# Performance work log

Hardware: AMD Instinct MI355X
Metric: run time of the kernel (lower is better)

The kernel has to match this reference:

```python
import jax, jax.numpy as jnp
import numpy as np
from jax import lax

B = 512
MBD_B, MBD_C = 64, 16
FEAT = 40 * 4 * 4  # 640


def _conv(x, w, b):
    y = lax.conv_general_dilated(x, w, (1, 1), 'VALID',
                                 dimension_numbers=('NCHW', 'OIHW', 'NCHW'))
    return y + b[None, :, None, None]


def _maxpool2(x):
    return lax.reduce_window(x, -jnp.inf, lax.max,
                             (1, 1, 2, 2), (1, 1, 2, 2), 'VALID')


def setup_inputs() -> dict:
    key = jax.random.key(0)
    ks = jax.random.split(key, 10)
    def he(k, shape, fan_in):
        return jax.random.normal(k, shape, dtype=jnp.float32) * np.float32(1.0 / np.sqrt(fan_in))
    return {
        'x': jax.random.normal(ks[0], (B, 1, 28, 28), dtype=jnp.float32),
        'conv1_w': he(ks[1], (20, 1, 5, 5), 25),
        'conv1_b': jnp.zeros((20,), jnp.float32),
        'conv2_w': he(ks[2], (40, 20, 5, 5), 20 * 25),
        'conv2_b': jnp.zeros((40,), jnp.float32),
        'T': he(ks[3], (MBD_B * MBD_C, FEAT), FEAT),          # feature_scan_tensor (no bias)
        'fc1_w': he(ks[4], (100, FEAT + MBD_B), FEAT + MBD_B),
        'fc1_b': jnp.zeros((100,), jnp.float32),
        'fc2_w': he(ks[5], (1, 100), 100),
        'fc2_b': jnp.zeros((1,), jnp.float32),
    }


def reference(x, conv1_w, conv1_b, conv2_w, conv2_b, T, fc1_w, fc1_b, fc2_w, fc2_b):
    # conv feature extractor: [B,1,28,28] -> [B,40,4,4]
    h = _maxpool2(jax.nn.relu(_conv(x, conv1_w, conv1_b)))
    h = _maxpool2(jax.nn.relu(_conv(h, conv2_w, conv2_b)))
    feats = h.reshape(h.shape[0], -1)  # [B, 640]

    # minibatch discrimination: M = feats @ T^T -> [B, b, c]
    M = (feats @ T.T).reshape(-1, MBD_B, MBD_C)
    # pairwise L1 over c: [B, B, b] (includes j==i diagonal = 0, exp(0)=1, as in original)
    dist = jnp.abs(M[:, None, :, :] - M[None, :, :, :]).sum(axis=3)
    closeness = jnp.exp(-dist).sum(axis=1)  # [B, b]

    out = jnp.concatenate([feats, closeness], axis=1)  # [B, 640+b]
    out = jax.nn.relu(out @ fc1_w.T + fc1_b)
    # Dropout(p=0.2) omitted (deterministic eval-mode reference)
    out = jax.nn.sigmoid(out @ fc2_w.T + fc2_b)  # [B, 1]
    return out
```

## Files before the change

kernel.cpp:

```cpp
#include <hip/hip_runtime.h>


typedef __attribute__((ext_vector_type(8))) short bf16x8;
typedef __attribute__((ext_vector_type(4))) float f32x4;

static __device__ __forceinline__ unsigned short f2bf(float x) {
  unsigned int u = __float_as_uint(x);
  unsigned int r = (u + 0x7fffu + ((u >> 16) & 1u)) >> 16;
  return (unsigned short)r;
}
static __device__ __forceinline__ float bf2f(unsigned short h) {
  return __uint_as_float(((unsigned int)h) << 16);
}

__global__ __launch_bounds__(256) void kP_prep(
    const float* __restrict__ c2w, const float* __restrict__ T,
    float* __restrict__ ws2, unsigned short* __restrict__ Th,
    unsigned short* __restrict__ Tl) {
  const int idx = blockIdx.x * 256 + threadIdx.x;
  if (idx < 655360) {
    const float v = T[idx];
    const unsigned short h = f2bf(v);
    Th[idx] = h;
    Tl[idx] = f2bf(v - bf2f(h));
  }
  if (idx < 32000) {
    const int ic = idx / 1600;
    const int r = idx - ic * 1600;
    const int tap = r >> 6;
    const int slot = r & 63;
    const int grp = slot >> 3;
    const int q = slot & 7;
    float val = 0.f;
    if (q < 5) val = c2w[(grp * 5 + q) * 500 + ic * 25 + tap];
    ws2[idx] = val;
  }
}

__global__ __launch_bounds__(256) void kC_conv(
    const float* __restrict__ x, const float* __restrict__ c1w,
    const float* __restrict__ c1b, const float* __restrict__ ws2,
    const float* __restrict__ c2b, float* __restrict__ feats,
    unsigned short* __restrict__ fh, unsigned short* __restrict__ fl) {
  __shared__ __align__(16) float img[2][784];
  __shared__ __align__(16) float h1s[2][2880];
  __shared__ float wl1[500];
  __shared__ float bl1[20];
  __shared__ float bl2[40];
  __shared__ __align__(16) float wl2[2][2][1600];
  __shared__ float mg[2][64][41];

  const int tid = threadIdx.x;
  const int slot = tid >> 7;
  const int lt = tid & 127;
  const int imgId = blockIdx.x * 2 + slot;

  {
    float4* dst = reinterpret_cast<float4*>(&img[0][0]);
    for (int t = tid; t < 392; t += 256) {
      const int which = t / 196;
      const int within = t - which * 196;
      dst[t] = reinterpret_cast<const float4*>(
          x + (blockIdx.x * 2 + which) * 784)[within];
    }
  }
  for (int t = tid; t < 500; t += 256) wl1[t] = c1w[t];
  if (tid < 20) bl1[tid] = c1b[tid];
  if (tid >= 64 && tid < 104) bl2[tid - 64] = c2b[tid - 64];
  __syncthreads();

  for (int qd = lt; qd < 720; qd += 128) {
    const int ch = qd / 36;
    const int rem = qd - ch * 36;
    const int py = rem / 3;
    const int qx = rem - py * 3;
    const int r0 = py * 2;
    const int c0 = qx * 8;
    float p[6][12];
#pragma unroll
    for (int r = 0; r < 6; ++r) {
      const float* ib = &img[slot][(r0 + r) * 28 + c0];
      const float4 a = *reinterpret_cast<const float4*>(ib);
      const float4 b = *reinterpret_cast<const float4*>(ib + 4);
      const float4 c = *reinterpret_cast<const float4*>(ib + 8);
      p[r][0] = a.x; p[r][1] = a.y; p[r][2] = a.z; p[r][3] = a.w;
      p[r][4] = b.x; p[r][5] = b.y; p[r][6] = b.z; p[r][7] = b.w;
      p[r][8] = c.x; p[r][9] = c.y; p[r][10] = c.z; p[r][11] = c.w;
    }
    float s[16];
#pragma unroll
    for (int u = 0; u < 16; ++u) s[u] = 0.f;
    const float* wc = &wl1[ch * 25];
#pragma unroll
    for (int ky = 0; ky < 5; ++ky) {
#pragma unroll
      for (int kx = 0; kx < 5; ++kx) {
        const float w = wc[ky * 5 + kx];
#pragma unroll
        for (int u = 0; u < 4; ++u) {
#pragma unroll
          for (int dy = 0; dy < 2; ++dy) {
#pragma unroll
            for (int dx = 0; dx < 2; ++dx) {
              s[u * 4 + dy * 2 + dx] += p[ky + dy][2 * u + dx + kx] * w;
            }
          }
        }
      }
    }
    const float bb = bl1[ch];
    float4 o;
    o.x = fmaxf(fmaxf(fmaxf(s[0], s[1]), fmaxf(s[2], s[3])) + bb, 0.f);
    o.y = fmaxf(fmaxf(fmaxf(s[4], s[5]), fmaxf(s[6], s[7])) + bb, 0.f);
    o.z = fmaxf(fmaxf(fmaxf(s[8], s[9]), fmaxf(s[10], s[11])) + bb, 0.f);
    o.w = fmaxf(fmaxf(fmaxf(s[12], s[13]), fmaxf(s[14], s[15])) + bb, 0.f);
    *reinterpret_cast<float4*>(&h1s[slot][ch * 144 + py * 12 + qx * 4]) = o;
  }

  {
    float4* wlf4 = reinterpret_cast<float4*>(&wl2[0][0][0]);
    const float4* wsf4 = reinterpret_cast<const float4*>(ws2);
#pragma unroll
    for (int k = 0; k < 4; ++k) {
      const int e = tid + k * 256;
      if (e < 800) {
        const int str = e / 400;
        const int i4 = e - str * 400;
        wlf4[(str * 2 + 0) * 400 + i4] = wsf4[(str * 10 + 0) * 400 + i4];
      }
    }
  }
  __syncthreads();

  const int h = lt >> 6;
  const int grp = (lt >> 3) & 7;
  const int pp = lt & 7;
  const int oy = (pp >> 1) * 2;
  const int ox = (pp & 1) * 4;
  float acc[5][8];
#pragma unroll
  for (int q = 0; q < 5; ++q)
#pragma unroll
    for (int u = 0; u < 8; ++u) acc[q][u] = 0.f;

  float4* wlf4 = reinterpret_cast<float4*>(&wl2[0][0][0]);
  const float4* wsf4 = reinterpret_cast<const float4*>(ws2);
  for (int s = 0; s < 10; ++s) {
    const int p0 = s & 1;
    float4 sv[4];
    if (s < 9) {
#pragma unroll
      for (int k = 0; k < 4; ++k) {
        const int e = tid + k * 256;
        if (e < 800) {
          const int str = e / 400;
          const int i4 = e - str * 400;
          sv[k] = wsf4[(str * 10 + s + 1) * 400 + i4];
        }
      }
    }
    const int ic = h * 10 + s;
    float p[6][8];
#pragma unroll
    for (int r = 0; r < 6; ++r) {
      const float* ib = &h1s[slot][ic * 144 + (oy + r) * 12 + ox];
      const float4 a = *reinterpret_cast<const float4*>(ib);
      const float4 b = *reinterpret_cast<const float4*>(ib + 4);
      p[r][0] = a.x; p[r][1] = a.y; p[r][2] = a.z; p[r][3] = a.w;
      p[r][4] = b.x; p[r][5] = b.y; p[r][6] = b.z; p[r][7] = b.w;
    }
    const float* wbase = &wl2[h][p0][0];
#pragma unroll
    for (int ky = 0; ky < 5; ++ky) {
#pragma unroll
      for (int kx = 0; kx < 5; ++kx) {
        const int tap = ky * 5 + kx;
        const float4 w4 =
            *reinterpret_cast<const float4*>(&wbase[tap * 64 + grp * 8]);
        const float w4b = wbase[tap * 64 + grp * 8 + 4];
#pragma unroll
        for (int pooled = 0; pooled < 2; ++pooled) {
#pragma unroll
          for (int dy = 0; dy < 2; ++dy) {
#pragma unroll
            for (int dx = 0; dx < 2; ++dx) {
              const int u = pooled * 4 + dy * 2 + dx;
              const float iv = p[ky + dy][pooled * 2 + dx + kx];
              acc[0][u] += iv * w4.x;
              acc[1][u] += iv * w4.y;
              acc[2][u] += iv * w4.z;
              acc[3][u] += iv * w4.w;
              acc[4][u] += iv * w4b;
            }
          }
        }
      }
    }
    if (s < 9) {
#pragma unroll
      for (int k = 0; k < 4; ++k) {
        const int e = tid + k * 256;
        if (e < 800) {
          const int str = e / 400;
          const int i4 = e - str * 400;
          wlf4[(str * 2 + ((s + 1) & 1)) * 400 + i4] = sv[k];
        }
      }
    }
    __syncthreads();
  }

  const int midx = (grp << 3) | pp;
  if (h == 1) {
#pragma unroll
    for (int q = 0; q < 5; ++q)
#pragma unroll
      for (int u = 0; u < 8; ++u) mg[slot][midx][q * 8 + u] = acc[q][u];
  }
  __syncthreads();
  if (h == 0) {
    const int pos0 = (pp >> 1) * 4 + (pp & 1) * 2;
#pragma unroll
    for (int q = 0; q < 5; ++q) {
      const int ch = grp * 5 + q;
      float a[8];
#pragma unroll
      for (int u = 0; u < 8; ++u) a[u] = acc[q][u] + mg[slot][midx][q * 8 + u];
      const float bb = bl2[ch];
      const float r0v =
          fmaxf(fmaxf(fmaxf(a[0], a[1]), fmaxf(a[2], a[3])) + bb, 0.f);
      const float r1v =
          fmaxf(fmaxf(fmaxf(a[4], a[5]), fmaxf(a[6], a[7])) + bb, 0.f);
      const int off = imgId * 640 + ch * 16 + pos0;
      *reinterpret_cast<float2*>(&feats[off]) = make_float2(r0v, r1v);
      const unsigned short h0 = f2bf(r0v), h1v = f2bf(r1v);
      ushort2 hv; hv.x = h0; hv.y = h1v;
      ushort2 lv;
      lv.x = f2bf(r0v - bf2f(h0));
      lv.y = f2bf(r1v - bf2f(h1v));
      *reinterpret_cast<ushort2*>(&fh[off]) = hv;
      *reinterpret_cast<ushort2*>(&fl[off]) = lv;
    }
  }
}

__global__ __launch_bounds__(256) void k3m_gemm(
    const unsigned short* __restrict__ fh, const unsigned short* __restrict__ fl,
    const unsigned short* __restrict__ Th, const unsigned short* __restrict__ Tl,
    float* __restrict__ M) {
  __shared__ short Ah[64][40];
  __shared__ short Al[64][40];
  __shared__ short Bh[64][40];
  __shared__ short Bl[64][40];
  const int tid = threadIdx.x;
  const int i0 = blockIdx.y * 64;
  const int j0 = blockIdx.x * 64;
  const int row = tid >> 2, kq = tid & 3;
  const int l = tid & 63, w = tid >> 6;
  const int fr = l & 15, kslot = (l >> 4) * 8;

  f32x4 acc[4];
#pragma unroll
  for (int js = 0; js < 4; ++js) acc[js] = (f32x4){0.f, 0.f, 0.f, 0.f};

  for (int k0 = 0; k0 < 640; k0 += 32) {
    const int ga = (i0 + row) * 640 + k0 + kq * 8;
    const int gb = (j0 + row) * 640 + k0 + kq * 8;
    const uint4 vah = *reinterpret_cast<const uint4*>(fh + ga);
    const uint4 val_ = *reinterpret_cast<const uint4*>(fl + ga);
    const uint4 vbh = *reinterpret_cast<const uint4*>(Th + gb);
    const uint4 vbl = *reinterpret_cast<const uint4*>(Tl + gb);
    __syncthreads();
    *reinterpret_cast<uint4*>(&Ah[row][kq * 8]) = vah;
    *reinterpret_cast<uint4*>(&Al[row][kq * 8]) = val_;
    *reinterpret_cast<uint4*>(&Bh[row][kq * 8]) = vbh;
    *reinterpret_cast<uint4*>(&Bl[row][kq * 8]) = vbl;
    __syncthreads();
    const bf16x8 aH = *reinterpret_cast<const bf16x8*>(&Ah[w * 16 + fr][kslot]);
    const bf16x8 aL = *reinterpret_cast<const bf16x8*>(&Al[w * 16 + fr][kslot]);
#pragma unroll
    for (int js = 0; js < 4; ++js) {
      const bf16x8 bH =
          *reinterpret_cast<const bf16x8*>(&Bh[js * 16 + fr][kslot]);
      const bf16x8 bL =
          *reinterpret_cast<const bf16x8*>(&Bl[js * 16 + fr][kslot]);
      acc[js] = __builtin_amdgcn_mfma_f32_16x16x32_bf16(aH, bH, acc[js], 0, 0, 0);
      acc[js] = __builtin_amdgcn_mfma_f32_16x16x32_bf16(aL, bH, acc[js], 0, 0, 0);
      acc[js] = __builtin_amdgcn_mfma_f32_16x16x32_bf16(aH, bL, acc[js], 0, 0, 0);
    }
  }
#pragma unroll
  for (int js = 0; js < 4; ++js) {
#pragma unroll
    for (int r = 0; r < 4; ++r) {
      M[(i0 + w * 16 + (l >> 4) * 4 + r) * 1024 + j0 + js * 16 + (l & 15)] =
          acc[js][r];
    }
  }
}

__global__ __launch_bounds__(256) void k4_mbd(const float* __restrict__ M,
                                              float* __restrict__ cp) {
  __shared__ float4 jb4[2][4][256];
  const int bid = blockIdx.x;
  const int ig = bid >> 4;
  const int jq = bid & 15;
  const int t = threadIdx.x;
  const int b = t & 63;
  const int g = t >> 6;
  const int i0 = ig * 16 + g * 4;
  const float4* Mf4 = reinterpret_cast<const float4*>(M);

  float4 mi[4][4];
#pragma unroll
  for (int u = 0; u < 4; ++u) {
#pragma unroll
    for (int q = 0; q < 4; ++q) mi[u][q] = Mf4[(i0 + u) * 256 + b * 4 + q];
  }
  const int wslot = (t >> 2) * 4 + ((t & 3) ^ ((t >> 3) & 3));
  {
#pragma unroll
    for (int k = 0; k < 4; ++k)
      jb4[0][k][wslot] = Mf4[(jq * 32 + k) * 256 + t];
  }
  __syncthreads();

  float acc[4] = {0.f, 0.f, 0.f, 0.f};
  const int xr = (b >> 1) & 3;
  for (int c = 0; c < 8; ++c) {
    float4 st[4];
    if (c < 7) {
#pragma unroll
      for (int k = 0; k < 4; ++k)
        st[k] = Mf4[(jq * 32 + (c + 1) * 4 + k) * 256 + t];
    }
    const int cbuf = c & 1;
#pragma unroll
    for (int jj = 0; jj < 4; ++jj) {
      const float4* rowp = jb4[cbuf][jj];
      float4 mj[4];
#pragma unroll
      for (int q = 0; q < 4; ++q) mj[q] = rowp[b * 4 + (q ^ xr)];
#pragma unroll
      for (int u = 0; u < 4; ++u) {
        float dist =
            fabsf(mi[u][0].x - mj[0].x) + fabsf(mi[u][0].y - mj[0].y) +
            fabsf(mi[u][0].z - mj[0].z) + fabsf(mi[u][0].w - mj[0].w) +
            fabsf(mi[u][1].x - mj[1].x) + fabsf(mi[u][1].y - mj[1].y) +
            fabsf(mi[u][1].z - mj[1].z) + fabsf(mi[u][1].w - mj[1].w) +
            fabsf(mi[u][2].x - mj[2].x) + fabsf(mi[u][2].y - mj[2].y) +
            fabsf(mi[u][2].z - mj[2].z) + fabsf(mi[u][2].w - mj[2].w) +
            fabsf(mi[u][3].x - mj[3].x) + fabsf(mi[u][3].y - mj[3].y) +
            fabsf(mi[u][3].z - mj[3].z) + fabsf(mi[u][3].w - mj[3].w);
        acc[u] += __expf(-dist);
      }
    }
    if (c < 7) {
#pragma unroll
      for (int k = 0; k < 4; ++k) jb4[(c + 1) & 1][k][wslot] = st[k];
    }
    __syncthreads();
  }
#pragma unroll
  for (int u = 0; u < 4; ++u)
    cp[(jq * 512 + i0 + u) * 64 + b] = acc[u];
}

__global__ __launch_bounds__(256) void k5_head(
    const float* __restrict__ feats, const float* __restrict__ cp,
    const float* __restrict__ w1, const float* __restrict__ b1,
    const float* __restrict__ w2, const float* __restrict__ b2,
    float* __restrict__ out) {
  __shared__ __align__(16) float v[704];
  __shared__ float hb[100];
  const int i = blockIdx.x;
  const int tid = threadIdx.x;
  float4* v4 = reinterpret_cast<float4*>(v);
  if (tid < 160)
    v4[tid] = reinterpret_cast<const float4*>(feats + i * 640)[tid];
  if (tid >= 192) {
    const int bb = tid - 192;
    float s = 0.f;
#pragma unroll
    for (int q = 0; q < 16; ++q) s += cp[(q * 512 + i) * 64 + bb];
    v[640 + bb] = s;
  }
  __syncthreads();
  const int wave = tid >> 6;
  const int lane = tid & 63;
  for (int r = wave; r < 100; r += 4) {
    const float4* wr = reinterpret_cast<const float4*>(w1 + r * 704);
    const float4 wa = wr[lane];
    const float4 wb = wr[lane + 64];
    const float4 va = v4[lane];
    const float4 vb = v4[lane + 64];
    float s = wa.x * va.x + wa.y * va.y + wa.z * va.z + wa.w * va.w +
              wb.x * vb.x + wb.y * vb.y + wb.z * vb.z + wb.w * vb.w;
    if (lane < 48) {
      const float4 wc = wr[lane + 128];
      const float4 vc = v4[lane + 128];
      s += wc.x * vc.x + wc.y * vc.y + wc.z * vc.z + wc.w * vc.w;
    }
#pragma unroll
    for (int off = 32; off; off >>= 1) s += __shfl_xor(s, off);
    if (lane == 0) hb[r] = fmaxf(s + b1[r], 0.f) * w2[r];
  }
  __syncthreads();
  if (tid < 64) {
    float s = hb[tid] + ((tid < 36) ? hb[tid + 64] : 0.f);
#pragma unroll
    for (int off = 32; off; off >>= 1) s += __shfl_xor(s, off);
    if (tid == 0) out[i] = 1.f / (1.f + __expf(-(s + b2[0])));
  }
}

extern "C" void kernel_launch(void* const* d_in, const int* in_sizes, int n_in,
                              void* d_out, int out_size, void* d_ws,
                              size_t ws_size, hipStream_t stream) {
  const float* x   = (const float*)d_in[0];
  const float* c1w = (const float*)d_in[1];
  const float* c1b = (const float*)d_in[2];
  const float* c2w = (const float*)d_in[3];
  const float* c2b = (const float*)d_in[4];
  const float* T   = (const float*)d_in[5];
  const float* f1w = (const float*)d_in[6];
  const float* f1b = (const float*)d_in[7];
  const float* f2w = (const float*)d_in[8];
  const float* f2b = (const float*)d_in[9];
  float* out = (float*)d_out;

  float* feats = (float*)d_ws;
  float* M     = feats + 327680;
  float* cp    = M + 524288;
  float* ws2   = cp + 524288;
  unsigned short* fh = (unsigned short*)(ws2 + 32000);
  unsigned short* fl = fh + 327680;
  unsigned short* Th = fl + 327680;
  unsigned short* Tl = Th + 655360;

  kP_prep<<<2560, 256, 0, stream>>>(c2w, T, ws2, Th, Tl);
  kC_conv<<<256, 256, 0, stream>>>(x, c1w, c1b, ws2, c2b, feats, fh, fl);
  k3m_gemm<<<dim3(16, 8), 256, 0, stream>>>(fh, fl, Th, Tl, M);
  k4_mbd<<<512, 256, 0, stream>>>(M, cp);
  k5_head<<<512, 256, 0, stream>>>(feats, cp, f1w, f1b, f2w, f2b, out);
}
```

Before: 175.8 us.

## Use one image per conv block and drop LDS tiling in MBD GEMM

The conv kernel now gives each block one image instead of two, and each thread computes one pooled output per channel group instead of two. This doubles the block count to 512 and lowers register pressure, trading that for more redundant weight staging in LDS. The GEMM drops shared-memory tiling: each wave loads its 16x16 fragments straight from global memory with a fully unrolled K loop over 512 blocks. That removes the barriers and increases parallelism, at the cost of reloading the same operand rows from cache across blocks.

```diff
diff --git a/kernel.cpp b/kernel.cpp
--- a/kernel.cpp
+++ b/kernel.cpp
@@ -42,34 +42,28 @@
     const float* __restrict__ c1b, const float* __restrict__ ws2,
     const float* __restrict__ c2b, float* __restrict__ feats,
     unsigned short* __restrict__ fh, unsigned short* __restrict__ fl) {
-  __shared__ __align__(16) float img[2][784];
-  __shared__ __align__(16) float h1s[2][2880];
+  __shared__ __align__(16) float img[784];
+  __shared__ __align__(16) float h1s[2880];
   __shared__ float wl1[500];
   __shared__ float bl1[20];
   __shared__ float bl2[40];
   __shared__ __align__(16) float wl2[2][2][1600];
-  __shared__ float mg[2][64][41];
+  __shared__ float mg[128][21];
 
   const int tid = threadIdx.x;
-  const int slot = tid >> 7;
-  const int lt = tid & 127;
-  const int imgId = blockIdx.x * 2 + slot;
+  const int imgId = blockIdx.x;
 
   {
-    float4* dst = reinterpret_cast<float4*>(&img[0][0]);
-    for (int t = tid; t < 392; t += 256) {
-      const int which = t / 196;
-      const int within = t - which * 196;
-      dst[t] = reinterpret_cast<const float4*>(
-          x + (blockIdx.x * 2 + which) * 784)[within];
-    }
+    float4* dst = reinterpret_cast<float4*>(img);
+    const float4* src = reinterpret_cast<const float4*>(x + imgId * 784);
+    for (int t = tid; t < 196; t += 256) dst[t] = src[t];
   }
   for (int t = tid; t < 500; t += 256) wl1[t] = c1w[t];
   if (tid < 20) bl1[tid] = c1b[tid];
   if (tid >= 64 && tid < 104) bl2[tid - 64] = c2b[tid - 64];
   __syncthreads();
 
-  for (int qd = lt; qd < 720; qd += 128) {
+  for (int qd = tid; qd < 720; qd += 256) {
     const int ch = qd / 36;
     const int rem = qd - ch * 36;
     const int py = rem / 3;
@@ -79,7 +73,7 @@
     float p[6][12];
 #pragma unroll
     for (int r = 0; r < 6; ++r) {
-      const float* ib = &img[slot][(r0 + r) * 28 + c0];
+      const float* ib = &img[(r0 + r) * 28 + c0];
       const float4 a = *reinterpret_cast<const float4*>(ib);
       const float4 b = *reinterpret_cast<const float4*>(ib + 4);
       const float4 c = *reinterpret_cast<const float4*>(ib + 8);
@@ -114,37 +108,33 @@
     o.y = fmaxf(fmaxf(fmaxf(s[4], s[5]), fmaxf(s[6], s[7])) + bb, 0.f);
     o.z = fmaxf(fmaxf(fmaxf(s[8], s[9]), fmaxf(s[10], s[11])) + bb, 0.f);
     o.w = fmaxf(fmaxf(fmaxf(s[12], s[13]), fmaxf(s[14], s[15])) + bb, 0.f);
-    *reinterpret_cast<float4*>(&h1s[slot][ch * 144 + py * 12 + qx * 4]) = o;
-  }
-
-  {
-    float4* wlf4 = reinterpret_cast<float4*>(&wl2[0][0][0]);
-    const float4* wsf4 = reinterpret_cast<const float4*>(ws2);
-#pragma unroll
-    for (int k = 0; k < 4; ++k) {
-      const int e = tid + k * 256;
-      if (e < 800) {
-        const int str = e / 400;
-        const int i4 = e - str * 400;
-        wlf4[(str * 2 + 0) * 400 + i4] = wsf4[(str * 10 + 0) * 400 + i4];
-      }
-    }
-  }
-  __syncthreads();
-
-  const int h = lt >> 6;
-  const int grp = (lt >> 3) & 7;
-  const int pp = lt & 7;
-  const int oy = (pp >> 1) * 2;
-  const int ox = (pp & 1) * 4;
-  float acc[5][8];
-#pragma unroll
-  for (int q = 0; q < 5; ++q)
-#pragma unroll
-    for (int u = 0; u < 8; ++u) acc[q][u] = 0.f;
+    *reinterpret_cast<float4*>(&h1s[ch * 144 + py * 12 + qx * 4]) = o;
+  }
 
   float4* wlf4 = reinterpret_cast<float4*>(&wl2[0][0][0]);
   const float4* wsf4 = reinterpret_cast<const float4*>(ws2);
+#pragma unroll
+  for (int k = 0; k < 4; ++k) {
+    const int e = tid + k * 256;
+    if (e < 800) {
+      const int str = e / 400;
+      const int i4 = e - str * 400;
+      wlf4[(str * 2 + 0) * 400 + i4] = wsf4[(str * 10 + 0) * 400 + i4];
+    }
+  }
+  __syncthreads();
+
+  const int h = tid >> 7;
+  const int grp = (tid >> 4) & 7;
+  const int pos = tid & 15;
+  const int oy = (pos >> 2) * 2;
+  const int ox = (pos & 3) * 2;
+  float acc[5][4];
+#pragma unroll
+  for (int q = 0; q < 5; ++q)
+#pragma unroll
+    for (int u = 0; u < 4; ++u) acc[q][u] = 0.f;
+
   for (int s = 0; s < 10; ++s) {
     const int p0 = s & 1;
     float4 sv[4];
@@ -160,14 +150,17 @@
       }
     }
     const int ic = h * 10 + s;
-    float p[6][8];
-#pragma unroll
-    for (int r = 0; r < 6; ++r) {
-      const float* ib = &h1s[slot][ic * 144 + (oy + r) * 12 + ox];
-      const float4 a = *reinterpret_cast<const float4*>(ib);
-      const float4 b = *reinterpret_cast<const float4*>(ib + 4);
-      p[r][0] = a.x; p[r][1] = a.y; p[r][2] = a.z; p[r][3] = a.w;
-      p[r][4] = b.x; p[r][5] = b.y; p[r][6] = b.z; p[r][7] = b.w;
+    float p[6][6];
+    {
+      const float* ib = &h1s[ic * 144 + oy * 12 + ox];
+#pragma unroll
+      for (int r = 0; r < 6; ++r) {
+        const float2 v0 = *reinterpret_cast<const float2*>(&ib[r * 12 + 0]);
+        const float2 v1 = *reinterpret_cast<const float2*>(&ib[r * 12 + 2]);
+        const float2 v2 = *reinterpret_cast<const float2*>(&ib[r * 12 + 4]);
+        p[r][0] = v0.x; p[r][1] = v0.y; p[r][2] = v1.x;
+        p[r][3] = v1.y; p[r][4] = v2.x; p[r][5] = v2.y;
+      }
     }
     const float* wbase = &wl2[h][p0][0];
 #pragma unroll
@@ -178,22 +171,20 @@
         const float4 w4 =
             *reinterpret_cast<const float4*>(&wbase[tap * 64 + grp * 8]);
         const float w4b = wbase[tap * 64 + grp * 8 + 4];
-#pragma unroll
-        for (int pooled = 0; pooled < 2; ++pooled) {
-#pragma unroll
-          for (int dy = 0; dy < 2; ++dy) {
-#pragma unroll
-            for (int dx = 0; dx < 2; ++dx) {
-              const int u = pooled * 4 + dy * 2 + dx;
-              const float iv = p[ky + dy][pooled * 2 + dx + kx];
-              acc[0][u] += iv * w4.x;
-              acc[1][u] += iv * w4.y;
-              acc[2][u] += iv * w4.z;
-              acc[3][u] += iv * w4.w;
-              acc[4][u] += iv * w4b;
-            }
-          }
-        }
+        const float i00 = p[ky][kx];
+        const float i01 = p[ky][kx + 1];
+        const float i10 = p[ky + 1][kx];
+        const float i11 = p[ky + 1][kx + 1];
+        acc[0][0] += i00 * w4.x; acc[0][1] += i01 * w4.x;
+        acc[0][2] += i10 * w4.x; acc[0][3] += i11 * w4.x;
+        acc[1][0] += i00 * w4.y; acc[1][1] += i01 * w4.y;
+        acc[1][2] += i10 * w4.y; acc[1][3] += i11 * w4.y;
+        acc[2][0] += i00 * w4.z; acc[2][1] += i01 * w4.z;
+        acc[2][2] += i10 * w4.z; acc[2][3] += i11 * w4.z;
+        acc[3][0] += i00 * w4.w; acc[3][1] += i01 * w4.w;
+        acc[3][2] += i10 * w4.w; acc[3][3] += i11 * w4.w;
+        acc[4][0] += i00 * w4b; acc[4][1] += i01 * w4b;
+        acc[4][2] += i10 * w4b; acc[4][3] += i11 * w4b;
       }
     }
     if (s < 9) {
@@ -210,36 +201,29 @@
     __syncthreads();
   }
 
-  const int midx = (grp << 3) | pp;
+  const int midx = grp * 16 + pos;
   if (h == 1) {
 #pragma unroll
     for (int q = 0; q < 5; ++q)
 #pragma unroll
-      for (int u = 0; u < 8; ++u) mg[slot][midx][q * 8 + u] = acc[q][u];
+      for (int u = 0; u < 4; ++u) mg[midx][q * 4 + u] = acc[q][u];
   }
   __syncthreads();
   if (h == 0) {
-    const int pos0 = (pp >> 1) * 4 + (pp & 1) * 2;
 #pragma unroll
     for (int q = 0; q < 5; ++q) {
       const int ch = grp * 5 + q;
-      float a[8];
-#pragma unroll
-      for (int u = 0; u < 8; ++u) a[u] = acc[q][u] + mg[slot][midx][q * 8 + u];
-      const float bb = bl2[ch];
+      const float a0 = acc[q][0] + mg[midx][q * 4 + 0];
+      const float a1 = acc[q][1] + mg[midx][q * 4 + 1];
+      const float a2 = acc[q][2] + mg[midx][q * 4 + 2];
+      const float a3 = acc[q][3] + mg[midx][q * 4 + 3];
       const float r0v =
-          fmaxf(fmaxf(fmaxf(a[0], a[1]), fmaxf(a[2], a[3])) + bb, 0.f);
-      const float r1v =
-          fmaxf(fmaxf(fmaxf(a[4], a[5]), fmaxf(a[6], a[7])) + bb, 0.f);
-      const int off = imgId * 640 + ch * 16 + pos0;
-      *reinterpret_cast<float2*>(&feats[off]) = make_float2(r0v, r1v);
-      const unsigned short h0 = f2bf(r0v), h1v = f2bf(r1v);
-      ushort2 hv; hv.x = h0; hv.y = h1v;
-      ushort2 lv;
-      lv.x = f2bf(r0v - bf2f(h0));
-      lv.y = f2bf(r1v - bf2f(h1v));
-      *reinterpret_cast<ushort2*>(&fh[off]) = hv;
-      *reinterpret_cast<ushort2*>(&fl[off]) = lv;
+          fmaxf(fmaxf(fmaxf(a0, a1), fmaxf(a2, a3)) + bl2[ch], 0.f);
+      const int off = imgId * 640 + ch * 16 + pos;
+      feats[off] = r0v;
+      const unsigned short h0 = f2bf(r0v);
+      fh[off] = h0;
+      fl[off] = f2bf(r0v - bf2f(h0));
     }
   }
 }
@@ -248,54 +232,31 @@
     const unsigned short* __restrict__ fh, const unsigned short* __restrict__ fl,
     const unsigned short* __restrict__ Th, const unsigned short* __restrict__ Tl,
     float* __restrict__ M) {
-  __shared__ short Ah[64][40];
-  __shared__ short Al[64][40];
-  __shared__ short Bh[64][40];
-  __shared__ short Bl[64][40];
   const int tid = threadIdx.x;
-  const int i0 = blockIdx.y * 64;
-  const int j0 = blockIdx.x * 64;
-  const int row = tid >> 2, kq = tid & 3;
-  const int l = tid & 63, w = tid >> 6;
-  const int fr = l & 15, kslot = (l >> 4) * 8;
-
-  f32x4 acc[4];
-#pragma unroll
-  for (int js = 0; js < 4; ++js) acc[js] = (f32x4){0.f, 0.f, 0.f, 0.f};
-
-  for (int k0 = 0; k0 < 640; k0 += 32) {
-    const int ga = (i0 + row) * 640 + k0 + kq * 8;
-    const int gb = (j0 + row) * 640 + k0 + kq * 8;
-    const uint4 vah = *reinterpret_cast<const uint4*>(fh + ga);
-    const uint4 val_ = *reinterpret_cast<const uint4*>(fl + ga);
-    const uint4 vbh = *reinterpret_cast<const uint4*>(Th + gb);
-    const uint4 vbl = *reinterpret_cast<const uint4*>(Tl + gb);
-    __syncthreads();
-    *reinterpret_cast<uint4*>(&Ah[row][kq * 8]) = vah;
-    *reinterpret_cast<uint4*>(&Al[row][kq * 8]) = val_;
-    *reinterpret_cast<uint4*>(&Bh[row][kq * 8]) = vbh;
-    *reinterpret_cast<uint4*>(&Bl[row][kq * 8]) = vbl;
-    __syncthreads();
-    const bf16x8 aH = *reinterpret_cast<const bf16x8*>(&Ah[w * 16 + fr][kslot]);
-    const bf16x8 aL = *reinterpret_cast<const bf16x8*>(&Al[w * 16 + fr][kslot]);
-#pragma unroll
-    for (int js = 0; js < 4; ++js) {
-      const bf16x8 bH =
-          *reinterpret_cast<const bf16x8*>(&Bh[js * 16 + fr][kslot]);
-      const bf16x8 bL =
-          *reinterpret_cast<const bf16x8*>(&Bl[js * 16 + fr][kslot]);
-      acc[js] = __builtin_amdgcn_mfma_f32_16x16x32_bf16(aH, bH, acc[js], 0, 0, 0);
-      acc[js] = __builtin_amdgcn_mfma_f32_16x16x32_bf16(aL, bH, acc[js], 0, 0, 0);
-      acc[js] = __builtin_amdgcn_mfma_f32_16x16x32_bf16(aH, bL, acc[js], 0, 0, 0);
-    }
-  }
-#pragma unroll
-  for (int js = 0; js < 4; ++js) {
-#pragma unroll
-    for (int r = 0; r < 4; ++r) {
-      M[(i0 + w * 16 + (l >> 4) * 4 + r) * 1024 + j0 + js * 16 + (l & 15)] =
-          acc[js][r];
-    }
+  const int w = tid >> 6;
+  const int l = tid & 63;
+  const int fr = l & 15;
+  const int hi = l >> 4;
+  const int if0 = blockIdx.x >> 4;
+  const int jf = (blockIdx.x & 15) * 4 + w;
+  const int abase = (if0 * 16 + fr) * 640 + hi * 8;
+  const int bbase = (jf * 16 + fr) * 640 + hi * 8;
+
+  f32x4 acc = (f32x4){0.f, 0.f, 0.f, 0.f};
+#pragma unroll
+  for (int kk = 0; kk < 20; ++kk) {
+    const int ko = kk * 32;
+    const bf16x8 aH = *reinterpret_cast<const bf16x8*>(fh + abase + ko);
+    const bf16x8 aL = *reinterpret_cast<const bf16x8*>(fl + abase + ko);
+    const bf16x8 bH = *reinterpret_cast<const bf16x8*>(Th + bbase + ko);
+    const bf16x8 bL = *reinterpret_cast<const bf16x8*>(Tl + bbase + ko);
+    acc = __builtin_amdgcn_mfma_f32_16x16x32_bf16(aH, bH, acc, 0, 0, 0);
+    acc = __builtin_amdgcn_mfma_f32_16x16x32_bf16(aL, bH, acc, 0, 0, 0);
+    acc = __builtin_amdgcn_mfma_f32_16x16x32_bf16(aH, bL, acc, 0, 0, 0);
+  }
+#pragma unroll
+  for (int r = 0; r < 4; ++r) {
+    M[(if0 * 16 + hi * 4 + r) * 1024 + jf * 16 + fr] = acc[r];
   }
 }
 
@@ -439,8 +400,8 @@
   unsigned short* Tl = Th + 655360;
 
   kP_prep<<<2560, 256, 0, stream>>>(c2w, T, ws2, Th, Tl);
-  kC_conv<<<256, 256, 0, stream>>>(x, c1w, c1b, ws2, c2b, feats, fh, fl);
-  k3m_gemm<<<dim3(16, 8), 256, 0, stream>>>(fh, fl, Th, Tl, M);
+  kC_conv<<<512, 256, 0, stream>>>(x, c1w, c1b, ws2, c2b, feats, fh, fl);
+  k3m_gemm<<<512, 256, 0, stream>>>(fh, fl, Th, Tl, M);
   k4_mbd<<<512, 256, 0, stream>>>(M, cp);
   k5_head<<<512, 256, 0, stream>>>(feats, cp, f1w, f1b, f2w, f2b, out);
 }
```

After: 178.0 us. Within noise of the previous version (+1.2%).
